# Optimization experiments

Hardware: AMD Instinct MI355X
Metric: run time of the kernel (lower is better)

Reference implementation:

```python
import jax, jax.numpy as jnp
import numpy as np

N = 50000        # n_nodes
E = 1600000      # n_edges (avg degree 32)
M = 8            # multiplicity of node irreps 8x0e + 8x1o
R = 8            # radial embedding dim
H = 8            # radial MLP hidden width
OUT_IRREPS = 6 * M   # 24x0e + 24x1o -> 48 irreps (MLP output width)
AVG_NEIGH = 32.0
SQRT3 = np.sqrt(3.0).astype(np.float32)


def setup_inputs() -> dict:
    key = jax.random.key(0)
    ks = jax.random.split(key, 7)
    node_feats = jax.random.normal(ks[0], (N, 4 * M), dtype=jnp.float32)      # [M scalars | M*3 vector comps]
    edge_features = jax.random.normal(ks[1], (E, 4), dtype=jnp.float32)       # SH l=0 (1) + l=1 (3)
    radial_embedding = jax.random.uniform(ks[2], (E, R), dtype=jnp.float32)
    senders = jax.random.randint(ks[3], (E,), 0, N, dtype=jnp.int32)
    receivers = jax.random.randint(ks[4], (E,), 0, N, dtype=jnp.int32)
    w1 = jax.random.normal(ks[5], (R, H), dtype=jnp.float32) / np.sqrt(R).astype(np.float32)
    w2 = jax.random.normal(ks[6], (H, OUT_IRREPS), dtype=jnp.float32) / np.sqrt(H).astype(np.float32)
    return {"node_feats": node_feats, "edge_features": edge_features,
            "radial_embedding": radial_embedding, "w1": w1, "w2": w2,
            "senders": senders, "receivers": receivers}


def reference(node_feats, edge_features, radial_embedding, w1, w2, senders, receivers):
    # 1) irregular gather: messages = node_feats[senders]
    msg = node_feats[senders]                       # [E, 4M]
    s = msg[:, :M]                                  # [E, M]   scalars (0e)
    v = msg[:, M:].reshape(-1, M, 3)                # [E, M, 3] vectors (1o)
    e0 = edge_features[:, :1]                       # [E, 1]   SH l=0
    e1 = edge_features[:, 1:4]                      # [E, 3]   SH l=1

    # 2) CG tensor product node x edge, filtered to irreps_out + '0e' (= 0e + 1o)
    tp0a = s * e0                                   # 0e x 0e -> 0e   [E, M]
    tp0b = jnp.einsum('emc,ec->em', v, e1) / SQRT3  # 1o x 1o -> 0e   [E, M]
    tp1a = s[:, :, None] * e1[:, None, :]           # 0e x 1o -> 1o   [E, M, 3]
    tp1b = v * e0[:, :, None]                       # 1o x 0e -> 1o   [E, M, 3]

    # 3) concatenate original (filtered) messages with tp output, regrouped: 3M x 0e + 3M x 1o
    scal = jnp.concatenate([s, tp0a, tp0b], axis=1)        # [E, 3M]
    vec = jnp.concatenate([v, tp1a, tp1b], axis=1)         # [E, 3M, 3]

    # 4) radial MLP (no bias, swish hidden, linear output) -> one weight per irrep
    w = jax.nn.swish(radial_embedding @ w1) @ w2           # [E, 6M]
    scal = scal * w[:, :3 * M]
    vec = vec * w[:, 3 * M:, None]                          # broadcast over 3 components

    messages = jnp.concatenate([scal, vec.reshape(vec.shape[0], -1)], axis=1)  # [E, 12M]

    # 5) scatter-add to receivers + neighbour normalization
    out = jax.ops.segment_sum(messages, receivers, num_segments=N)             # [N, 12M]
    return out / np.sqrt(AVG_NEIGH).astype(np.float32)
```

## Files before the change

kernel.cpp:

```cpp
#include <hip/hip_runtime.h>


#define CAPACITY 96
#define CH 16

typedef _Float16 half2v __attribute__((ext_vector_type(2)));

__device__ __forceinline__ unsigned pk16(float a, float b) {
    return __builtin_bit_cast(unsigned, __builtin_amdgcn_cvt_pkrtz(a, b));
}

__device__ __forceinline__ float dot2h(unsigned a, half2v b, float c) {
#if __has_builtin(__builtin_amdgcn_fdot2)
    return __builtin_amdgcn_fdot2(__builtin_bit_cast(half2v, a), b, c, false);
#else
    half2v av = __builtin_bit_cast(half2v, a);
    return fmaf((float)av.x, (float)b.x, fmaf((float)av.y, (float)b.y, c));
#endif
}

__global__ __launch_bounds__(256) void hist_kernel(
    const int* __restrict__ recv, int* __restrict__ cnt, int E)
{
    int e = blockIdx.x * 256 + threadIdx.x;
    if (e < E) atomicAdd(&cnt[recv[e]], 1);
}

__global__ __launch_bounds__(1024) void scan_kernel(
    const int* __restrict__ cnt, int* __restrict__ off,
    int* __restrict__ cursor, int N)
{
    __shared__ int lds[1024];
    const int t = threadIdx.x;
    const int CHN = (N + 1023) / 1024;
    const int lo = t * CHN;
    const int hi = min(N, lo + CHN);
    int s = 0;
    for (int i = lo; i < hi; ++i) s += cnt[i];
    lds[t] = s;
    __syncthreads();
    for (int d = 1; d < 1024; d <<= 1) {
        int v = (t >= d) ? lds[t - d] : 0;
        __syncthreads();
        lds[t] += v;
        __syncthreads();
    }
    int run = (t > 0) ? lds[t - 1] : 0;
    for (int i = lo; i < hi; ++i) {
        off[i] = run;
        cursor[i] = run;
        run += cnt[i];
    }
    if (t == 1023) off[N] = lds[1023];
}

__global__ __launch_bounds__(256) void build_recs_kernel(
    const float* __restrict__ edge_features,
    const float* __restrict__ radial,
    const float* __restrict__ w1g,
    const int* __restrict__ senders,
    const int* __restrict__ recv,
    int* __restrict__ slots,
    uint4* __restrict__ recs,
    int E, int CAP)
{
    __shared__ float sw1[64];
    for (int i = threadIdx.x; i < 64; i += 256) sw1[i] = w1g[i];
    __syncthreads();

    int e = blockIdx.x * 256 + threadIdx.x;
    if (e >= E) return;

    const int rcv_ = recv[e];
    size_t addr;
    if (CAP > 0) {
        int slot = atomicAdd(&slots[rcv_], 1);
        slot = min(slot, CAP - 1);
        addr = (size_t)rcv_ * CAP + slot;
    } else {
        addr = (size_t)atomicAdd(&slots[rcv_], 1);
    }

    const float4 ef = reinterpret_cast<const float4*>(edge_features)[e];
    const float4 ra = reinterpret_cast<const float4*>(radial)[2 * e + 0];
    const float4 rb = reinterpret_cast<const float4*>(radial)[2 * e + 1];
    const int snd = senders[e];

    float r[8] = {ra.x, ra.y, ra.z, ra.w, rb.x, rb.y, rb.z, rb.w};
    float h[8];
#pragma unroll
    for (int j = 0; j < 8; ++j) {
        float x = 0.f;
#pragma unroll
        for (int i = 0; i < 8; ++i) x = fmaf(r[i], sw1[i * 8 + j], x);
        h[j] = 0.17677669529663687f * x * __builtin_amdgcn_rcpf(1.0f + __expf(-x));
    }

    uint4 qa, qb;
    qa.x = pk16(h[0], h[1]); qa.y = pk16(h[2], h[3]);
    qa.z = pk16(h[4], h[5]); qa.w = pk16(h[6], h[7]);
    qb.x = pk16(ef.x, ef.y); qb.y = pk16(ef.z, ef.w);
    qb.z = (unsigned)snd;    qb.w = 0u;
    recs[2 * addr + 0] = qa;
    recs[2 * addr + 1] = qb;
}

template<bool CAPMODE>
__global__ __launch_bounds__(256) void node_v12_kernel(
    const float* __restrict__ node_feats,
    const float* __restrict__ w2g,
    const int* __restrict__ off,
    const uint4* __restrict__ recs,
    float* __restrict__ out,
    int N)
{
    const int lane = threadIdx.x & 63;
    const int wv   = threadIdx.x >> 6;
    const int node = blockIdx.x * 4 + wv;

    __shared__ uint4 rec_lds[4][CH][2];
    __shared__ float nf_lds[4][CH][32];
    __shared__ float scr[4][128];

    int kA, iA, selA; float scA = 1.0f;
    if (lane < 8)       { kA = lane;         iA = lane;     selA = 0; }
    else if (lane < 16) { kA = lane;         iA = lane - 8; selA = 1; }
    else if (lane < 40) { int t = lane - 16; kA = 16 + t / 3; iA = 8 + t;
                          selA = 2 + t % 3;  scA = 0.57735026918962576f; }
    else                { int t = lane - 40; kA = 24 + t / 3; iA = 8 + t; selA = 0; }

    int kB, iB, selB; const bool deadB = (lane >= 48);
    if (lane < 24)      { int t = lane;      kB = 32 + t / 3; iB = t / 3; selB = 2 + t % 3; }
    else if (lane < 48) { int t = lane - 24; kB = 40 + t / 3; iB = 8 + t; selB = 1; }
    else                { kB = 0; iB = 0; selB = 0; }

    half2v wpA[4], wpB[4];
#pragma unroll
    for (int i = 0; i < 4; ++i) {
        wpA[i].x = (_Float16)(w2g[(2 * i + 0) * 48 + kA] * scA);
        wpA[i].y = (_Float16)(w2g[(2 * i + 1) * 48 + kA] * scA);
        wpB[i].x = deadB ? (_Float16)0.f : (_Float16)(w2g[(2 * i + 0) * 48 + kB]);
        wpB[i].y = deadB ? (_Float16)0.f : (_Float16)(w2g[(2 * i + 1) * 48 + kB]);
    }

    if (node >= N) return;

    int base, count;
    if (CAPMODE) { base = node * CAPACITY; count = min(off[node], CAPACITY); }
    else         { base = off[node];       count = off[node + 1] - base; }
    const uint4* rp = recs + (size_t)base * 2;

    const int r_stage = lane >> 2;
    const int q_stage = lane & 3;

    float acc0 = 0.f, acc1 = 0.f;

    for (int c0i = 0; c0i < count; c0i += CH) {
        const int cc = min(CH, count - c0i);

        if (lane < 2 * cc)
            rec_lds[wv][lane >> 1][lane & 1] = rp[(size_t)c0i * 2 + lane];

        if (r_stage < cc) {
            const unsigned snd =
                reinterpret_cast<const unsigned*>(rp)[((size_t)c0i + r_stage) * 8 + 6];
            const float4* src = reinterpret_cast<const float4*>(node_feats)
                                + (size_t)snd * 8 + q_stage * 2;
            const float4 v0 = src[0];
            const float4 v1 = src[1];
            float4* dst = reinterpret_cast<float4*>(&nf_lds[wv][r_stage][q_stage * 8]);
            dst[0] = v0;
            dst[1] = v1;
        }

#pragma unroll 4
        for (int i = 0; i < cc; ++i) {
            const uint4 qa = rec_lds[wv][i][0];
            const uint2 eq = *reinterpret_cast<const uint2*>(&rec_lds[wv][i][1]);

            float wAv = dot2h(qa.x, wpA[0], 0.f);
            wAv = dot2h(qa.y, wpA[1], wAv);
            wAv = dot2h(qa.z, wpA[2], wAv);
            wAv = dot2h(qa.w, wpA[3], wAv);
            float wBv = dot2h(qa.x, wpB[0], 0.f);
            wBv = dot2h(qa.y, wpB[1], wBv);
            wBv = dot2h(qa.z, wpB[2], wBv);
            wBv = dot2h(qa.w, wpB[3], wBv);

            const half2v eA = __builtin_bit_cast(half2v, eq.x);
            const half2v eB = __builtin_bit_cast(half2v, eq.y);
            const float e0  = (float)eA.x, e1x = (float)eA.y;
            const float e1y = (float)eB.x, e1z = (float)eB.y;

            const float n0 = nf_lds[wv][i][iA];
            const float n1 = nf_lds[wv][i][iB];

            const float fA = (selA == 0) ? 1.0f
                           : (selA == 1) ? e0
                           : (selA == 2) ? e1x
                           : (selA == 3) ? e1y : e1z;
            const float fB = (selB == 1) ? e0
                           : (selB == 2) ? e1x
                           : (selB == 3) ? e1y : e1z;

            acc0 = fmaf(wAv, n0 * fA, acc0);
            acc1 = fmaf(wBv, n1 * fB, acc1);
        }
    }

    scr[wv][lane]      = acc0;
    scr[wv][64 + lane] = acc1;
    float o0;
    if (lane < 16) {
        o0 = scr[wv][lane];
    } else if (lane < 24) {
        const int t = 16 + 3 * (lane - 16);
        o0 = scr[wv][t] + scr[wv][t + 1] + scr[wv][t + 2];
    } else {
        o0 = scr[wv][lane + 16];
    }
    float* orow = out + (size_t)node * 96;
    orow[lane] = o0;
    if (lane < 32) orow[64 + lane] = scr[wv][80 + lane];
}

extern "C" void kernel_launch(void* const* d_in, const int* in_sizes, int n_in,
                              void* d_out, int out_size, void* d_ws, size_t ws_size,
                              hipStream_t stream) {
    const float* node_feats    = (const float*)d_in[0];
    const float* edge_features = (const float*)d_in[1];
    const float* radial        = (const float*)d_in[2];
    const float* w1            = (const float*)d_in[3];
    const float* w2            = (const float*)d_in[4];
    const int*   senders       = (const int*)d_in[5];
    const int*   receivers     = (const int*)d_in[6];
    float* out = (float*)d_out;

    const int E = in_sizes[5];
    const int N = out_size / 96;
    const int eblocks = (E + 255) / 256;
    const int nblocks = (N + 3) / 4;

    const size_t needP1 = (size_t)N * CAPACITY * 32 + (size_t)N * sizeof(int);

    if (ws_size >= needP1) {
        uint4* recs = (uint4*)d_ws;
        int* cnt = (int*)((char*)d_ws + (size_t)N * CAPACITY * 32);

        (void)hipMemsetAsync(cnt, 0, (size_t)N * sizeof(int), stream);
        hipLaunchKernelGGL(build_recs_kernel, dim3(eblocks), dim3(256), 0, stream,
                           edge_features, radial, w1, senders, receivers,
                           cnt, recs, E, CAPACITY);
        hipLaunchKernelGGL(node_v12_kernel<true>, dim3(nblocks), dim3(256), 0, stream,
                           node_feats, w2, cnt, recs, out, N);
    } else {
        uint4* recs = (uint4*)d_ws;
        int* cnt    = (int*)((char*)d_ws + (size_t)E * 32);
        int* off    = cnt + N;
        int* cursor = cnt + 2 * N + 1;

        (void)hipMemsetAsync(cnt, 0, (size_t)N * sizeof(int), stream);
        hipLaunchKernelGGL(hist_kernel, dim3(eblocks), dim3(256), 0, stream,
                           receivers, cnt, E);
        hipLaunchKernelGGL(scan_kernel, dim3(1), dim3(1024), 0, stream,
                           cnt, off, cursor, N);
        hipLaunchKernelGGL(build_recs_kernel, dim3(eblocks), dim3(256), 0, stream,
                           edge_features, radial, w1, senders, receivers,
                           cursor, recs, E, 0);
        hipLaunchKernelGGL(node_v12_kernel<false>, dim3(nblocks), dim3(256), 0, stream,
                           node_feats, w2, off, recs, out, N);
    }
}
```

Measured before the change: 325.1 us.

## Pad per-node atomic counters, select edge factors via fp16 dot masks, pad LDS rows

Per-node slot counters are spread to a 64-byte stride (16 ints) so that atomics from different receivers no longer share cache lines, provided the workspace is large enough. The edge record now stores a constant 1.0 alongside the edge features, which lets each lane pick its edge factor with three masked fp16 dot2 ops instead of a per-lane select chain. The node-feature LDS rows are padded from 32 to 36 floats to reduce bank conflicts. In exchange the counter memset grows 16x, and the factor selection costs extra dot instructions in the inner loop.

```diff
diff --git a/kernel.cpp b/kernel.cpp
--- a/kernel.cpp
+++ b/kernel.cpp
@@ -62,7 +62,7 @@
     const int* __restrict__ recv,
     int* __restrict__ slots,
     uint4* __restrict__ recs,
-    int E, int CAP)
+    int E, int CAP, int cstr)
 {
     __shared__ float sw1[64];
     for (int i = threadIdx.x; i < 64; i += 256) sw1[i] = w1g[i];
@@ -74,7 +74,7 @@
     const int rcv_ = recv[e];
     size_t addr;
     if (CAP > 0) {
-        int slot = atomicAdd(&slots[rcv_], 1);
+        int slot = atomicAdd(&slots[(size_t)rcv_ * cstr], 1);
         slot = min(slot, CAP - 1);
         addr = (size_t)rcv_ * CAP + slot;
     } else {
@@ -99,14 +99,16 @@
     uint4 qa, qb;
     qa.x = pk16(h[0], h[1]); qa.y = pk16(h[2], h[3]);
     qa.z = pk16(h[4], h[5]); qa.w = pk16(h[6], h[7]);
-    qb.x = pk16(ef.x, ef.y); qb.y = pk16(ef.z, ef.w);
-    qb.z = (unsigned)snd;    qb.w = 0u;
+    qb.x = pk16(1.0f, ef.x);
+    qb.y = pk16(ef.y, ef.z);
+    qb.z = (unsigned)snd;
+    qb.w = pk16(ef.w, 0.0f);
     recs[2 * addr + 0] = qa;
     recs[2 * addr + 1] = qb;
 }
 
-template<bool CAPMODE>
-__global__ __launch_bounds__(256) void node_v12_kernel(
+template<bool CAPMODE, int CSTR>
+__global__ __launch_bounds__(256) void node_v14_kernel(
     const float* __restrict__ node_feats,
     const float* __restrict__ w2g,
     const int* __restrict__ off,
@@ -119,7 +121,7 @@
     const int node = blockIdx.x * 4 + wv;
 
     __shared__ uint4 rec_lds[4][CH][2];
-    __shared__ float nf_lds[4][CH][32];
+    __shared__ float nf_lds[4][CH][36];
     __shared__ float scr[4][128];
 
     int kA, iA, selA; float scA = 1.0f;
@@ -133,6 +135,20 @@
     if (lane < 24)      { int t = lane;      kB = 32 + t / 3; iB = t / 3; selB = 2 + t % 3; }
     else if (lane < 48) { int t = lane - 24; kB = 40 + t / 3; iB = 8 + t; selB = 1; }
     else                { kB = 0; iB = 0; selB = 0; }
+
+    half2v mA0 = {0, 0}, mA1 = {0, 0}, mA2 = {0, 0};
+    if      (selA == 0) mA0.x = (_Float16)1.f;
+    else if (selA == 1) mA0.y = (_Float16)1.f;
+    else if (selA == 2) mA1.x = (_Float16)1.f;
+    else if (selA == 3) mA1.y = (_Float16)1.f;
+    else                mA2.x = (_Float16)1.f;
+    half2v mB0 = {0, 0}, mB1 = {0, 0}, mB2 = {0, 0};
+    if (!deadB) {
+        if      (selB == 1) mB0.y = (_Float16)1.f;
+        else if (selB == 2) mB1.x = (_Float16)1.f;
+        else if (selB == 3) mB1.y = (_Float16)1.f;
+        else                mB2.x = (_Float16)1.f;
+    }
 
     half2v wpA[4], wpB[4];
 #pragma unroll
@@ -146,7 +162,7 @@
     if (node >= N) return;
 
     int base, count;
-    if (CAPMODE) { base = node * CAPACITY; count = min(off[node], CAPACITY); }
+    if (CAPMODE) { base = node * CAPACITY; count = min(off[(size_t)node * CSTR], CAPACITY); }
     else         { base = off[node];       count = off[node + 1] - base; }
     const uint4* rp = recs + (size_t)base * 2;
 
@@ -168,15 +184,15 @@
                                 + (size_t)snd * 8 + q_stage * 2;
             const float4 v0 = src[0];
             const float4 v1 = src[1];
-            float4* dst = reinterpret_cast<float4*>(&nf_lds[wv][r_stage][q_stage * 8]);
-            dst[0] = v0;
-            dst[1] = v1;
+            float* dst = &nf_lds[wv][r_stage][q_stage * 8];
+            *reinterpret_cast<float4*>(dst)     = v0;
+            *reinterpret_cast<float4*>(dst + 4) = v1;
         }
 
 #pragma unroll 4
         for (int i = 0; i < cc; ++i) {
             const uint4 qa = rec_lds[wv][i][0];
-            const uint2 eq = *reinterpret_cast<const uint2*>(&rec_lds[wv][i][1]);
+            const uint4 qb = rec_lds[wv][i][1];
 
             float wAv = dot2h(qa.x, wpA[0], 0.f);
             wAv = dot2h(qa.y, wpA[1], wAv);
@@ -187,21 +203,15 @@
             wBv = dot2h(qa.z, wpB[2], wBv);
             wBv = dot2h(qa.w, wpB[3], wBv);
 
-            const half2v eA = __builtin_bit_cast(half2v, eq.x);
-            const half2v eB = __builtin_bit_cast(half2v, eq.y);
-            const float e0  = (float)eA.x, e1x = (float)eA.y;
-            const float e1y = (float)eB.x, e1z = (float)eB.y;
+            float fA = dot2h(qb.x, mA0, 0.f);
+            fA = dot2h(qb.y, mA1, fA);
+            fA = dot2h(qb.w, mA2, fA);
+            float fB = dot2h(qb.x, mB0, 0.f);
+            fB = dot2h(qb.y, mB1, fB);
+            fB = dot2h(qb.w, mB2, fB);
 
             const float n0 = nf_lds[wv][i][iA];
             const float n1 = nf_lds[wv][i][iB];
-
-            const float fA = (selA == 0) ? 1.0f
-                           : (selA == 1) ? e0
-                           : (selA == 2) ? e1x
-                           : (selA == 3) ? e1y : e1z;
-            const float fB = (selB == 1) ? e0
-                           : (selB == 2) ? e1x
-                           : (selB == 3) ? e1y : e1z;
 
             acc0 = fmaf(wAv, n0 * fA, acc0);
             acc1 = fmaf(wBv, n1 * fB, acc1);
@@ -241,17 +251,29 @@
     const int eblocks = (E + 255) / 256;
     const int nblocks = (N + 3) / 4;
 
-    const size_t needP1 = (size_t)N * CAPACITY * 32 + (size_t)N * sizeof(int);
-
-    if (ws_size >= needP1) {
+    const size_t recsBytes = (size_t)N * CAPACITY * 32;
+    const size_t needPad   = recsBytes + (size_t)N * 16 * sizeof(int);
+    const size_t needP1    = recsBytes + (size_t)N * sizeof(int);
+
+    if (ws_size >= needPad) {
         uint4* recs = (uint4*)d_ws;
-        int* cnt = (int*)((char*)d_ws + (size_t)N * CAPACITY * 32);
+        int* cnt = (int*)((char*)d_ws + recsBytes);
+
+        (void)hipMemsetAsync(cnt, 0, (size_t)N * 16 * sizeof(int), stream);
+        hipLaunchKernelGGL(build_recs_kernel, dim3(eblocks), dim3(256), 0, stream,
+                           edge_features, radial, w1, senders, receivers,
+                           cnt, recs, E, CAPACITY, 16);
+        hipLaunchKernelGGL((node_v14_kernel<true, 16>), dim3(nblocks), dim3(256), 0, stream,
+                           node_feats, w2, cnt, recs, out, N);
+    } else if (ws_size >= needP1) {
+        uint4* recs = (uint4*)d_ws;
+        int* cnt = (int*)((char*)d_ws + recsBytes);
 
         (void)hipMemsetAsync(cnt, 0, (size_t)N * sizeof(int), stream);
         hipLaunchKernelGGL(build_recs_kernel, dim3(eblocks), dim3(256), 0, stream,
                            edge_features, radial, w1, senders, receivers,
-                           cnt, recs, E, CAPACITY);
-        hipLaunchKernelGGL(node_v12_kernel<true>, dim3(nblocks), dim3(256), 0, stream,
+                           cnt, recs, E, CAPACITY, 1);
+        hipLaunchKernelGGL((node_v14_kernel<true, 1>), dim3(nblocks), dim3(256), 0, stream,
                            node_feats, w2, cnt, recs, out, N);
     } else {
         uint4* recs = (uint4*)d_ws;
@@ -266,8 +288,8 @@
                            cnt, off, cursor, N);
         hipLaunchKernelGGL(build_recs_kernel, dim3(eblocks), dim3(256), 0, stream,
                            edge_features, radial, w1, senders, receivers,
-                           cursor, recs, E, 0);
-        hipLaunchKernelGGL(node_v12_kernel<false>, dim3(nblocks), dim3(256), 0, stream,
+                           cursor, recs, E, 0, 1);
+        hipLaunchKernelGGL((node_v14_kernel<false, 1>), dim3(nblocks), dim3(256), 0, stream,
                            node_feats, w2, off, recs, out, N);
     }
 }
```

Measured after the change: 308.0 us. 5.2% less time.
